# Kernel optimization log

Measured on AMD Instinct MI355X. Metric: run time of the kernel, lower is better.

The kernel has to match this reference:

```python
import jax, jax.numpy as jnp
import numpy as np

D_MODEL = 512
NHEAD = 8
HEAD_DIM = D_MODEL // NHEAD
LN_EPS = 1e-5


def layer_norm(x, gamma, beta):
    mu = jnp.mean(x, axis=-1, keepdims=True)
    var = jnp.var(x, axis=-1, keepdims=True)
    return (x - mu) * jax.lax.rsqrt(var + LN_EPS) * gamma + beta


def setup_inputs() -> dict:
    key = jax.random.key(0)
    ks = jax.random.split(key, 10)
    B, L, S = 2, 4096, 4096
    d = D_MODEL
    s = 0.02
    return {
        "x": jax.random.normal(ks[0], (B, L, d), dtype=jnp.float32),
        "source": jax.random.normal(ks[1], (B, S, d), dtype=jnp.float32),
        "Wq": jax.random.normal(ks[2], (d, d), dtype=jnp.float32) * s,
        "Wk": jax.random.normal(ks[3], (d, d), dtype=jnp.float32) * s,
        "Wv": jax.random.normal(ks[4], (d, d), dtype=jnp.float32) * s,
        "Wm": jax.random.normal(ks[5], (d, d), dtype=jnp.float32) * s,
        "W1": jax.random.normal(ks[6], (2 * d, 2 * d), dtype=jnp.float32) * s,
        "W2": jax.random.normal(ks[7], (d, 2 * d), dtype=jnp.float32) * s,
        "g1": jnp.ones((d,), dtype=jnp.float32),
        "b1": jnp.zeros((d,), dtype=jnp.float32),
        "g2": jnp.ones((d,), dtype=jnp.float32),
        "b2": jnp.zeros((d,), dtype=jnp.float32),
    }


def reference(x, source, Wq, Wk, Wv, Wm, W1, W2, g1, b1, g2, b2):
    bs, L, _ = x.shape
    S = source.shape[1]
    # projections (torch Linear: y = x @ W^T), split into heads
    qw = (x @ Wq.T).reshape(bs, L, NHEAD, HEAD_DIM)
    kw = (source @ Wk.T).reshape(bs, S, NHEAD, HEAD_DIM)
    vw = (source @ Wv.T).reshape(bs, S, NHEAD, HEAD_DIM)
    # attention scores [B, L, S, H], softmax over S (axis=2)
    a = jnp.einsum('nlhd,nshd->nlsh', qw, kw) / jnp.sqrt(jnp.float32(HEAD_DIM))
    a = jax.nn.softmax(a, axis=2)
    o = jnp.einsum('nlsh,nshd->nlhd', a, vw).reshape(bs, L, NHEAD * HEAD_DIM)
    message = layer_norm(o @ Wm.T, g1, b1)
    h = jnp.concatenate([x, message], axis=2)  # [B, L, 2D]
    h = jax.nn.relu(h @ W1.T) @ W2.T
    message = layer_norm(h, g2, b2)
    return x + message
```

## Files before the change

### kernel.cpp

```cpp
#include <hip/hip_runtime.h>
#include <stdint.h>

typedef short bh8 __attribute__((ext_vector_type(8)));
typedef float fx4 __attribute__((ext_vector_type(4)));
typedef float fx16 __attribute__((ext_vector_type(16)));
typedef unsigned short u16;
typedef unsigned int u32;
typedef u32 u32x4 __attribute__((ext_vector_type(4)));
typedef u16 us4 __attribute__((ext_vector_type(4)));

#define NHEAD 8
#define HD 64
#define DM 512
#define SEQ 4096
#define ROWS 8192
#define CEXP 0.1803368801111244f

#define MODE_BF16 1
#define MODE_RELU_BF16 2
#define MODE_KV 3

__device__ __forceinline__ u16 f2bf(float f) {
  union { float f; u32 u; } x; x.f = f;
  u32 u = x.u;
  u = u + 0x7fffu + ((u >> 16) & 1u);
  return (u16)(u >> 16);
}
__device__ __forceinline__ float bf2f(u16 h) {
  union { u32 u; float f; } x; x.u = ((u32)h) << 16;
  return x.f;
}
__device__ __forceinline__ void gll16(const void* g, void* l) {
  __builtin_amdgcn_global_load_lds(
      (const __attribute__((address_space(1))) void*)(uintptr_t)g,
      (__attribute__((address_space(3))) void*)(uintptr_t)l,
      16, 0, 0);
}
__device__ __forceinline__ fx4 mfma16(bh8 a, bh8 b, fx4 c) {
  return __builtin_amdgcn_mfma_f32_16x16x32_bf16(a, b, c, 0, 0, 0);
}
__device__ __forceinline__ fx16 mfma32(bh8 a, bh8 b, fx16 c) {
  return __builtin_amdgcn_mfma_f32_32x32x16_bf16(a, b, c, 0, 0, 0);
}
__device__ __forceinline__ u32 cvtpk(float lo, float hi) {
  u32 r; asm("v_cvt_pk_bf16_f32 %0, %1, %2" : "=v"(r) : "v"(lo), "v"(hi));
  return r;
}
__device__ __forceinline__ void pswap(u32& a, u32& b) {
  auto r = __builtin_amdgcn_permlane32_swap(a, b, false, false);
  a = r[0]; b = r[1];
}

__device__ __forceinline__ int fragidx4(int n, int k4, int K) {
  return (((((n >> 4) * (K >> 5) + (k4 >> 5)) << 2) + ((k4 >> 3) & 3)) * 16 + (n & 15)) * 2
         + ((k4 & 7) >> 2);
}

__global__ __launch_bounds__(256) void cvt_all_kernel(
    const float* __restrict__ x, const float* __restrict__ src,
    const float* __restrict__ Wq, const float* __restrict__ Wk,
    const float* __restrict__ Wv, const float* __restrict__ Wm,
    const float* __restrict__ W1, const float* __restrict__ W2,
    u16* __restrict__ xb, u16* __restrict__ sb,
    u16* __restrict__ wqb, u16* __restrict__ wkvb, u16* __restrict__ wmb,
    u16* __restrict__ w1b, u16* __restrict__ w2b) {
  const int NQ = ROWS * DM / 4;
  const int TOT = 2 * NQ + 655360;
  for (int i = blockIdx.x * 256 + threadIdx.x; i < TOT; i += gridDim.x * 256) {
    const float* s; u16* d; int j; int widx = -1;
    if (i < NQ)            { s = x;  d = xb;  j = i; }
    else if (i < 2 * NQ)   { s = src; d = sb; j = i - NQ; }
    else {
      int k = i - 2 * NQ;
      int n, k4, K;
      if (k < 65536)       { s = Wq; d = wqb; j = k;          n = j >> 7; k4 = (j & 127) << 2; K = 512; }
      else if (k < 131072) { s = Wk; d = wkvb; j = k - 65536; n = j >> 7; k4 = (j & 127) << 2; K = 512; }
      else if (k < 196608) { s = Wv; d = wkvb; j = k - 131072; n = (j >> 7) + 512; k4 = (j & 127) << 2; K = 512; }
      else if (k < 262144) { s = Wm; d = wmb; j = k - 196608; n = j >> 7; k4 = (j & 127) << 2; K = 512; }
      else if (k < 524288) { s = W1; d = w1b; j = k - 262144; n = j >> 8; k4 = (j & 255) << 2; K = 1024; }
      else                 { s = W2; d = w2b; j = k - 524288; n = j >> 8; k4 = (j & 255) << 2; K = 1024; }
      widx = fragidx4(n, k4, K);
    }
    float4 v = ((const float4*)s)[j];
    us4 o; o.x = f2bf(v.x); o.y = f2bf(v.y); o.z = f2bf(v.z); o.w = f2bf(v.w);
    ((us4*)d)[widx < 0 ? j : widx] = o;
  }
}

template <int NTW>
__device__ __forceinline__ void gemm_core(
    char* smem, const u16* __restrict__ A, const u16* __restrict__ A2, int strideA,
    const u16* __restrict__ Bw, void* __restrict__ Cp, void* __restrict__ C2p,
    int N, int K, int mode, float scl, int bx, int by) {
  const int tid = threadIdx.x;
  const int w = tid >> 6, l = tid & 63;
  const int fr = l & 15, fg = l >> 4;
  const int row0 = by * 128, col0 = bx * NTW * 32;
  const int wr = (w >> 1) * 64, wc = (w & 1) * NTW * 16;

  auto STAGE = [&](int buf, int k0) {
    const u16* Asrc = (k0 < 512) ? A : A2;
    const int kk = k0 & (strideA - 1);
    char* dst = smem + buf * 16384;
#pragma unroll
    for (int i = 0; i < 4; i++) {
      int t = i * 256 + tid;
      int rr = t >> 3, g = t & 7;
      int gs = g ^ (rr & 7);
      gll16(Asrc + (size_t)(row0 + rr) * strideA + kk + gs * 8, dst + i * 4096 + w * 1024);
    }
  };

  fx4 acc[4][NTW];
#pragma unroll
  for (int m = 0; m < 4; m++)
#pragma unroll
    for (int n = 0; n < NTW; n++)
#pragma unroll
      for (int r = 0; r < 4; r++) acc[m][n][r] = 0.f;

  STAGE(0, 0);
  __syncthreads();

  const int nk = K / 64;
  for (int ti = 0; ti < nk; ti++) {
    const int k0 = ti * 64;
    bh8 bfr[2][NTW];
#pragma unroll
    for (int ks = 0; ks < 2; ks++)
#pragma unroll
      for (int n = 0; n < NTW; n++) {
        const u16* bp = Bw +
            ((((size_t)((col0 + wc) >> 4) + n) * (K >> 5) + (k0 >> 5) + ks) * 4 + fg) * 128 +
            fr * 8;
        bfr[ks][n] = *(const bh8*)bp;
      }
    if (ti + 1 < nk) STAGE((ti + 1) & 1, k0 + 64);
    const char* sA = smem + (ti & 1) * 16384;
#pragma unroll
    for (int ks = 0; ks < 2; ks++) {
      bh8 af[4];
#pragma unroll
      for (int m = 0; m < 4; m++) {
        int rr = wr + m * 16 + fr;
        af[m] = *(const bh8*)(sA + rr * 128 + ((ks * 64 + fg * 16) ^ ((rr & 7) << 4)));
      }
      __builtin_amdgcn_s_setprio(1);
#pragma unroll
      for (int m = 0; m < 4; m++)
#pragma unroll
        for (int n = 0; n < NTW; n++) acc[m][n] = mfma16(af[m], bfr[ks][n], acc[m][n]);
      __builtin_amdgcn_s_setprio(0);
    }
    __syncthreads();
  }
#pragma unroll
  for (int m = 0; m < 4; m++)
#pragma unroll
    for (int n = 0; n < NTW; n++)
#pragma unroll
      for (int r = 0; r < 4; r++) {
        int row = row0 + wr + m * 16 + fg * 4 + r;
        int col = col0 + wc + n * 16 + fr;
        float v = acc[m][n][r];
        if (mode == MODE_BF16) {
          ((u16*)Cp)[(size_t)row * N + col] = f2bf(v * scl);
        } else if (mode == MODE_RELU_BF16) {
          ((u16*)Cp)[(size_t)row * N + col] = f2bf(v > 0.f ? v : 0.f);
        } else {
          int bb = row >> 12, s = row & 4095;
          if (col < 512) {
            int h = col >> 6, dd = col & 63;
            ((u16*)Cp)[(((size_t)((bb * 8 + h) * 8 + (dd >> 3))) * SEQ + s) * 8 + (dd & 7)] = f2bf(v);
          } else {
            int dd2 = col - 512;
            int h = dd2 >> 6, dd = dd2 & 63;
            ((u16*)C2p)[(((size_t)((bb * 8 + h) * 512 + (s >> 3))) * 64 + dd) * 8 + (s & 7)] = f2bf(v);
          }
        }
      }
}

__global__ __launch_bounds__(256) void qkv_kernel(
    const u16* __restrict__ xb, const u16* __restrict__ sb,
    const u16* __restrict__ wqb, const u16* __restrict__ wkvb,
    u16* __restrict__ Qb, u16* __restrict__ K2, u16* __restrict__ V2) {
  __shared__ __attribute__((aligned(16))) char smem[2 * 16384];
  int bid = blockIdx.x;
  if (bid < 256) {
    gemm_core<4>(smem, xb, xb, 512, wqb, Qb, nullptr, 512, 512, MODE_BF16, CEXP,
                 bid >> 6, bid & 63);
  } else {
    int kb = bid - 256;
    gemm_core<4>(smem, sb, sb, 512, wkvb, K2, V2, 1024, 512, MODE_KV, 1.0f,
                 kb >> 6, kb & 63);
  }
}

__global__ __launch_bounds__(256) void ffn1_kernel(
    const u16* __restrict__ xb, const u16* __restrict__ m0ln,
    const u16* __restrict__ w1b, u16* __restrict__ h1) {
  __shared__ __attribute__((aligned(16))) char smem[2 * 16384];
  int bid = blockIdx.x;
  gemm_core<4>(smem, xb, m0ln, 512, w1b, h1, nullptr, 1024, 1024, MODE_RELU_BF16, 1.0f,
               bid >> 6, bid & 63);
}

__global__ __launch_bounds__(256) void gemm64_kernel(
    const u16* __restrict__ A, const u16* __restrict__ A2, int strideA,
    const u16* __restrict__ Bw, u16* __restrict__ Cp, int K, float scl) {
  __shared__ __attribute__((aligned(16))) char smem[2 * 16384];
  int bid = blockIdx.x;
  gemm_core<2>(smem, A, A2, strideA, Bw, Cp, nullptr, 512, K, MODE_BF16, scl,
               bid >> 6, bid & 63);
}

__global__ __launch_bounds__(256, 3) void attn_kernel(
    const u16* __restrict__ Q, const u16* __restrict__ K2,
    const u16* __restrict__ V2, u16* __restrict__ O) {
  const int tid = threadIdx.x;
  const int w = tid >> 6, l = tid & 63;
  const int l31 = l & 31, hi = l >> 5;

  int dl = blockIdx.x;
  int c = dl & 7, j = dl >> 3;
  int bh = 2 * c + (j >> 5);
  int qb = j & 31;
  const int b = bh >> 3, h = bh & 7;
  const int qr0 = b * SEQ + qb * 128 + w * 32;
  const int NT = SEQ / 64;

  bh8 qf[4];
#pragma unroll
  for (int ks = 0; ks < 4; ks++)
    qf[ks] = *(const bh8*)(Q + (size_t)(qr0 + l31) * DM + h * HD + ks * 16 + hi * 8);

  const u16* Kbase = K2 + (size_t)bh * 8 * SEQ * 8;
  const u16* Vbase = V2 + (size_t)bh * 512 * 64 * 8;

  const u16* kp[4]; const u16* vp[4];
#pragma unroll
  for (int ks = 0; ks < 4; ks++) {
    kp[ks] = Kbase + ((size_t)(ks * 2 + hi) * SEQ + l31) * 8;
    vp[ks] = Vbase + ((size_t)(ks * 2 + hi) * 64 + l31) * 8;
  }

  fx16 o0, o1;
#pragma unroll
  for (int r = 0; r < 16; r++) { o0[r] = 0.f; o1[r] = 0.f; }
  float l_run = 0.f;

  for (int t = 0; t < NT; ++t) {
    bh8 kf0[4], kf1[4];
#pragma unroll
    for (int ks = 0; ks < 4; ks++) {
      kf0[ks] = *(const bh8*)kp[ks];
      kf1[ks] = *(const bh8*)(kp[ks] + 256);
    }

    fx16 s0v, s1v;
#pragma unroll
    for (int r = 0; r < 16; r++) { s0v[r] = 0.f; s1v[r] = 0.f; }
    __builtin_amdgcn_s_setprio(1);
#pragma unroll
    for (int ks = 0; ks < 4; ks++) {
      s0v = mfma32(kf0[ks], qf[ks], s0v);
      s1v = mfma32(kf1[ks], qf[ks], s1v);
    }
    __builtin_amdgcn_s_setprio(0);

    bh8 vf0[4], vf1[4];
#pragma unroll
    for (int ks = 0; ks < 4; ks++) {
      vf0[ks] = *(const bh8*)vp[ks];
      vf1[ks] = *(const bh8*)(vp[ks] + 256);
    }
#pragma unroll
    for (int ks = 0; ks < 4; ks++) { kp[ks] += 512; vp[ks] += 4096; }

    float rs = 0.f;
#pragma unroll
    for (int r = 0; r < 16; r++) {
      s0v[r] = __builtin_amdgcn_exp2f(s0v[r]); rs += s0v[r];
    }
#pragma unroll
    for (int r = 0; r < 16; r++) {
      s1v[r] = __builtin_amdgcn_exp2f(s1v[r]); rs += s1v[r];
    }
    l_run += rs;

    __builtin_amdgcn_s_setprio(1);
#pragma unroll
    for (int ks = 0; ks < 4; ks++) {
      int o8 = (ks & 1) * 8;
      u32 w0a, w1a, w0b, w1b;
      if (ks < 2) {
        w0a = cvtpk(s0v[o8 + 0], s0v[o8 + 1]);
        w1a = cvtpk(s0v[o8 + 2], s0v[o8 + 3]);
        w0b = cvtpk(s0v[o8 + 4], s0v[o8 + 5]);
        w1b = cvtpk(s0v[o8 + 6], s0v[o8 + 7]);
      } else {
        w0a = cvtpk(s1v[o8 + 0], s1v[o8 + 1]);
        w1a = cvtpk(s1v[o8 + 2], s1v[o8 + 3]);
        w0b = cvtpk(s1v[o8 + 4], s1v[o8 + 5]);
        w1b = cvtpk(s1v[o8 + 6], s1v[o8 + 7]);
      }
      pswap(w0a, w0b); pswap(w1a, w1b);
      u32x4 fw; fw.x = w0a; fw.y = w1a; fw.z = w0b; fw.w = w1b;
      bh8 pa = __builtin_bit_cast(bh8, fw);
      o0 = mfma32(pa, vf0[ks], o0);
      o1 = mfma32(pa, vf1[ks], o1);
    }
    __builtin_amdgcn_s_setprio(0);
  }

  l_run += __shfl_xor(l_run, 32);
#pragma unroll
  for (int r = 0; r < 16; r++) {
    int crow = (r & 3) + 8 * (r >> 2) + 4 * hi;
    float li = 1.0f / __shfl(l_run, crow);
    size_t row = (size_t)(qr0 + crow);
    O[row * DM + h * HD + l31] = f2bf(o0[r] * li);
    O[row * DM + h * HD + 32 + l31] = f2bf(o1[r] * li);
  }
}

__global__ __launch_bounds__(256) void ln_kernel(
    const u16* __restrict__ M0, const float* __restrict__ g1,
    const float* __restrict__ b1, u16* __restrict__ out) {
  const int row = blockIdx.x * 4 + (threadIdx.x >> 6);
  const int lane = threadIdx.x & 63;
  bh8 v = *(const bh8*)(M0 + (size_t)row * 512 + lane * 8);
  float f[8], s = 0.f, s2 = 0.f;
#pragma unroll
  for (int j = 0; j < 8; j++) { f[j] = bf2f((u16)v[j]); s += f[j]; s2 += f[j] * f[j]; }
#pragma unroll
  for (int off = 1; off <= 32; off <<= 1) {
    s += __shfl_xor(s, off);
    s2 += __shfl_xor(s2, off);
  }
  float mu = s * (1.f / 512.f);
  float var = s2 * (1.f / 512.f) - mu * mu;
  float rstd = rsqrtf(var + 1e-5f);
  int col = lane * 8;
  bh8 o;
#pragma unroll
  for (int j = 0; j < 8; j++)
    o[j] = (short)f2bf((f[j] - mu) * rstd * g1[col + j] + b1[col + j]);
  *(bh8*)(out + (size_t)row * 512 + col) = o;
}

__global__ __launch_bounds__(256) void ln_res_kernel(
    const u16* __restrict__ F, const float* __restrict__ X,
    const float* __restrict__ g2, const float* __restrict__ b2,
    float* __restrict__ out) {
  const int row = blockIdx.x * 4 + (threadIdx.x >> 6);
  const int lane = threadIdx.x & 63;
  bh8 v = *(const bh8*)(F + (size_t)row * 512 + lane * 8);
  float f[8], s = 0.f, s2 = 0.f;
#pragma unroll
  for (int j = 0; j < 8; j++) { f[j] = bf2f((u16)v[j]); s += f[j]; s2 += f[j] * f[j]; }
#pragma unroll
  for (int off = 1; off <= 32; off <<= 1) {
    s += __shfl_xor(s, off);
    s2 += __shfl_xor(s2, off);
  }
  float mu = s * (1.f / 512.f);
  float var = s2 * (1.f / 512.f) - mu * mu;
  float rstd = rsqrtf(var + 1e-5f);
  int col = lane * 8;
  const float* xr = X + (size_t)row * 512 + col;
  float* orow = out + (size_t)row * 512 + col;
#pragma unroll
  for (int j = 0; j < 8; j++)
    orow[j] = xr[j] + (f[j] - mu) * rstd * g2[col + j] + b2[col + j];
}

extern "C" void kernel_launch(void* const* d_in, const int* in_sizes, int n_in,
                              void* d_out, int out_size, void* d_ws, size_t ws_size,
                              hipStream_t stream) {
  (void)in_sizes; (void)n_in; (void)out_size; (void)ws_size;
  const float* x   = (const float*)d_in[0];
  const float* src = (const float*)d_in[1];
  const float* Wq  = (const float*)d_in[2];
  const float* Wk  = (const float*)d_in[3];
  const float* Wv  = (const float*)d_in[4];
  const float* Wm  = (const float*)d_in[5];
  const float* W1  = (const float*)d_in[6];
  const float* W2  = (const float*)d_in[7];
  const float* g1  = (const float*)d_in[8];
  const float* b1  = (const float*)d_in[9];
  const float* g2  = (const float*)d_in[10];
  const float* b2  = (const float*)d_in[11];

  char* ws = (char*)d_ws;
  u16* xb   = (u16*)(ws + 0);
  u16* sb   = (u16*)(ws + 8388608);
  u16* wqb  = (u16*)(ws + 16777216);
  u16* wkvb = (u16*)(ws + 17301504);
  u16* wmb  = (u16*)(ws + 18350080);
  u16* w1b  = (u16*)(ws + 18874368);
  u16* w2b  = (u16*)(ws + 20971520);
  u16* Qb   = (u16*)(ws + 22020096);
  u16* K2b  = (u16*)(ws + 30408704);
  u16* V2b  = (u16*)(ws + 38797312);
  u16* Ob   = (u16*)(ws + 47185920);

  u16* M0b  = (u16*)(ws + 30408704);
  u16* m0ln = (u16*)(ws + 38797312);
  u16* h1b  = (u16*)(ws + 22020096);
  u16* fb   = (u16*)(ws + 8388608);

  cvt_all_kernel<<<2048, 256, 0, stream>>>(x, src, Wq, Wk, Wv, Wm, W1, W2,
                                           xb, sb, wqb, wkvb, wmb, w1b, w2b);
  qkv_kernel<<<768, 256, 0, stream>>>(xb, sb, wqb, wkvb, Qb, K2b, V2b);
  attn_kernel<<<512, 256, 0, stream>>>(Qb, K2b, V2b, Ob);
  gemm64_kernel<<<512, 256, 0, stream>>>(Ob, Ob, 512, wmb, M0b, 512, 1.0f);
  ln_kernel<<<2048, 256, 0, stream>>>(M0b, g1, b1, m0ln);
  ffn1_kernel<<<512, 256, 0, stream>>>(xb, m0ln, w1b, h1b);
  gemm64_kernel<<<512, 256, 0, stream>>>(h1b, h1b, 1024, w2b, fb, 1024, 1.0f);
  ln_res_kernel<<<2048, 256, 0, stream>>>(fb, x, g2, b2, (float*)d_out);
}
```

Before: 190.3 us.

## Double-buffer K/V fragments in registers across attention tiles

The attention loop now prefetches the next tile's K and V fragments into a second register set while the current tile's QK^T, exp and PV MFMAs run, alternating two buffers across an unrolled pair of iterations. The goal is to hide global-load latency behind MFMA and exp work instead of relying only on wave occupancy. To make room for the extra registers, launch bounds drop from 3 to 2 waves per SIMD, which reduces the latency hiding that comes from occupancy. The final iteration also prefetches one tile past the end of each head's K/V slice, an unused read that can run past the buffer for the last head.

```diff
diff --git a/kernel.cpp b/kernel.cpp
--- a/kernel.cpp
+++ b/kernel.cpp
@@ -215,7 +215,7 @@
                bid >> 6, bid & 63);
 }
 
-__global__ __launch_bounds__(256, 3) void attn_kernel(
+__global__ __launch_bounds__(256, 2) void attn_kernel(
     const u16* __restrict__ Q, const u16* __restrict__ K2,
     const u16* __restrict__ V2, u16* __restrict__ O) {
   const int tid = threadIdx.x;
@@ -250,69 +250,79 @@
   for (int r = 0; r < 16; r++) { o0[r] = 0.f; o1[r] = 0.f; }
   float l_run = 0.f;
 
-  for (int t = 0; t < NT; ++t) {
-    bh8 kf0[4], kf1[4];
-#pragma unroll
-    for (int ks = 0; ks < 4; ks++) {
-      kf0[ks] = *(const bh8*)kp[ks];
-      kf1[ks] = *(const bh8*)(kp[ks] + 256);
-    }
-
-    fx16 s0v, s1v;
-#pragma unroll
-    for (int r = 0; r < 16; r++) { s0v[r] = 0.f; s1v[r] = 0.f; }
-    __builtin_amdgcn_s_setprio(1);
-#pragma unroll
-    for (int ks = 0; ks < 4; ks++) {
-      s0v = mfma32(kf0[ks], qf[ks], s0v);
-      s1v = mfma32(kf1[ks], qf[ks], s1v);
-    }
-    __builtin_amdgcn_s_setprio(0);
-
-    bh8 vf0[4], vf1[4];
-#pragma unroll
-    for (int ks = 0; ks < 4; ks++) {
-      vf0[ks] = *(const bh8*)vp[ks];
-      vf1[ks] = *(const bh8*)(vp[ks] + 256);
-    }
-#pragma unroll
-    for (int ks = 0; ks < 4; ks++) { kp[ks] += 512; vp[ks] += 4096; }
-
-    float rs = 0.f;
-#pragma unroll
-    for (int r = 0; r < 16; r++) {
-      s0v[r] = __builtin_amdgcn_exp2f(s0v[r]); rs += s0v[r];
-    }
-#pragma unroll
-    for (int r = 0; r < 16; r++) {
-      s1v[r] = __builtin_amdgcn_exp2f(s1v[r]); rs += s1v[r];
-    }
-    l_run += rs;
-
-    __builtin_amdgcn_s_setprio(1);
-#pragma unroll
-    for (int ks = 0; ks < 4; ks++) {
-      int o8 = (ks & 1) * 8;
-      u32 w0a, w1a, w0b, w1b;
-      if (ks < 2) {
-        w0a = cvtpk(s0v[o8 + 0], s0v[o8 + 1]);
-        w1a = cvtpk(s0v[o8 + 2], s0v[o8 + 3]);
-        w0b = cvtpk(s0v[o8 + 4], s0v[o8 + 5]);
-        w1b = cvtpk(s0v[o8 + 6], s0v[o8 + 7]);
-      } else {
-        w0a = cvtpk(s1v[o8 + 0], s1v[o8 + 1]);
-        w1a = cvtpk(s1v[o8 + 2], s1v[o8 + 3]);
-        w0b = cvtpk(s1v[o8 + 4], s1v[o8 + 5]);
-        w1b = cvtpk(s1v[o8 + 6], s1v[o8 + 7]);
-      }
-      pswap(w0a, w0b); pswap(w1a, w1b);
-      u32x4 fw; fw.x = w0a; fw.y = w1a; fw.z = w0b; fw.w = w1b;
-      bh8 pa = __builtin_bit_cast(bh8, fw);
-      o0 = mfma32(pa, vf0[ks], o0);
-      o1 = mfma32(pa, vf1[ks], o1);
-    }
-    __builtin_amdgcn_s_setprio(0);
-  }
+  bh8 kA0[4], kA1[4], vA0[4], vA1[4];
+  bh8 kB0[4], kB1[4], vB0[4], vB1[4];
+
+#pragma unroll
+  for (int ks = 0; ks < 4; ks++) {
+    kA0[ks] = *(const bh8*)kp[ks];
+    kA1[ks] = *(const bh8*)(kp[ks] + 256);
+    vA0[ks] = *(const bh8*)vp[ks];
+    vA1[ks] = *(const bh8*)(vp[ks] + 256);
+    kp[ks] += 512; vp[ks] += 4096;
+  }
+
+#define ATTN_TILE(kf0, kf1, vf0, vf1, nk0, nk1, nv0, nv1)                      \
+  {                                                                            \
+                \
+    _Pragma("unroll")                                                          \
+    for (int ks = 0; ks < 4; ks++) {                                           \
+      nk0[ks] = *(const bh8*)kp[ks];                                           \
+      nk1[ks] = *(const bh8*)(kp[ks] + 256);                                   \
+      nv0[ks] = *(const bh8*)vp[ks];                                           \
+      nv1[ks] = *(const bh8*)(vp[ks] + 256);                                   \
+      kp[ks] += 512; vp[ks] += 4096;                                           \
+    }                                                                          \
+    fx16 s0v, s1v;                                                             \
+    _Pragma("unroll")                                                          \
+    for (int r = 0; r < 16; r++) { s0v[r] = 0.f; s1v[r] = 0.f; }               \
+    __builtin_amdgcn_s_setprio(1);                                             \
+    _Pragma("unroll")                                                          \
+    for (int ks = 0; ks < 4; ks++) {                                           \
+      s0v = mfma32(kf0[ks], qf[ks], s0v);                                      \
+      s1v = mfma32(kf1[ks], qf[ks], s1v);                                      \
+    }                                                                          \
+    __builtin_amdgcn_s_setprio(0);                                             \
+    float rs = 0.f;                                                            \
+    _Pragma("unroll")                                                          \
+    for (int r = 0; r < 16; r++) {                                             \
+      s0v[r] = __builtin_amdgcn_exp2f(s0v[r]); rs += s0v[r];                   \
+    }                                                                          \
+    _Pragma("unroll")                                                          \
+    for (int r = 0; r < 16; r++) {                                             \
+      s1v[r] = __builtin_amdgcn_exp2f(s1v[r]); rs += s1v[r];                   \
+    }                                                                          \
+    l_run += rs;                                                               \
+    __builtin_amdgcn_s_setprio(1);                                             \
+    _Pragma("unroll")                                                          \
+    for (int ks = 0; ks < 4; ks++) {                                           \
+      int o8 = (ks & 1) * 8;                                                   \
+      u32 w0a, w1a, w0b, w1b;                                                  \
+      if (ks < 2) {                                                            \
+        w0a = cvtpk(s0v[o8 + 0], s0v[o8 + 1]);                                 \
+        w1a = cvtpk(s0v[o8 + 2], s0v[o8 + 3]);                                 \
+        w0b = cvtpk(s0v[o8 + 4], s0v[o8 + 5]);                                 \
+        w1b = cvtpk(s0v[o8 + 6], s0v[o8 + 7]);                                 \
+      } else {                                                                 \
+        w0a = cvtpk(s1v[o8 + 0], s1v[o8 + 1]);                                 \
+        w1a = cvtpk(s1v[o8 + 2], s1v[o8 + 3]);                                 \
+        w0b = cvtpk(s1v[o8 + 4], s1v[o8 + 5]);                                 \
+        w1b = cvtpk(s1v[o8 + 6], s1v[o8 + 7]);                                 \
+      }                                                                        \
+      pswap(w0a, w0b); pswap(w1a, w1b);                                        \
+      u32x4 fw; fw.x = w0a; fw.y = w1a; fw.z = w0b; fw.w = w1b;                \
+      bh8 pa = __builtin_bit_cast(bh8, fw);                                    \
+      o0 = mfma32(pa, vf0[ks], o0);                                            \
+      o1 = mfma32(pa, vf1[ks], o1);                                            \
+    }                                                                          \
+    __builtin_amdgcn_s_setprio(0);                                             \
+  }
+
+  for (int t = 0; t < NT; t += 2) {
+    ATTN_TILE(kA0, kA1, vA0, vA1, kB0, kB1, vB0, vB1)
+    ATTN_TILE(kB0, kB1, vB0, vB1, kA0, kA1, vA0, vA1)
+  }
+#undef ATTN_TILE
 
   l_run += __shfl_xor(l_run, 32);
 #pragma unroll
```

Result: slower. 194.3 us (+2.1%).
